# Optimization experiments

Measured on AMD Instinct MI355X. Metric: run time of the kernel, lower is better.

The kernel has to match this reference:

```python
import jax, jax.numpy as jnp
import numpy as np

N, D, L, K = 128, 512, 512, 512


def setup_inputs() -> dict:
    key = jax.random.key(0)
    k1, k2 = jax.random.split(key, 2)
    x = jax.random.normal(k1, (N, D, L), dtype=jnp.float32)
    a = jnp.ones((D,), dtype=jnp.float32) * 0.5
    sigma = jax.random.uniform(k2, (D,), dtype=jnp.float32)
    return {"x": x, "a": a, "sigma": sigma}


def reference(x, a, sigma):
    # x: (N, D, L); a, sigma: (D,)
    Lf = x.shape[-1]
    n = jnp.arange(Lf, dtype=x.dtype)                      # (L,)
    k = jnp.arange(K, dtype=x.dtype)                       # (K,)
    denom = jnp.asarray(Lf - 1, dtype=x.dtype)
    # Hann-family window per feature: w[d,l] = a[d] - (1-a[d]) cos(2*pi*l/(L-1))
    window = a[:, None] - (1.0 - a)[:, None] * jnp.cos(n * (2.0 * jnp.pi) / denom)  # (D, L)
    # windowed + sigma-scaled signal (fused elementwise)
    xw = x * (window * jnp.exp(sigma / denom)[:, None])    # (N, D, L)
    # complex DFT basis exp(j*2*pi*l*k/(L-1)) split into real/imag GEMMs
    ang = (2.0 * jnp.pi / denom) * (n[:, None] * k[None, :])  # (L, K)
    Xr = jnp.einsum('ndl,lk->ndk', xw, jnp.cos(ang))
    Xi = jnp.einsum('ndl,lk->ndk', xw, jnp.sin(ang))
    # abs_flag=True -> magnitude spectrum
    return jnp.sqrt(Xr * Xr + Xi * Xi)                     # (N, D, K)
```

## Files before the change

### kernel.cpp

```cpp
#include <hip/hip_runtime.h>
#include <hip/hip_bf16.h>
#include <math.h>

#define N_  128
#define D_  512
#define L_  512
#define K_  512
#define KH_ 256
#define M_  (N_*D_)

typedef __bf16 bf16x8 __attribute__((ext_vector_type(8)));
typedef float  f32x4  __attribute__((ext_vector_type(4)));
typedef unsigned short ushort_t;

__global__ void basis_kernel(const float* __restrict__ a,
                             const float* __restrict__ sigma,
                             ushort_t* __restrict__ Bc,
                             ushort_t* __restrict__ Bs,
                             float* __restrict__ P,
                             float* __restrict__ Q,
                             float* __restrict__ C) {
    int idx = blockIdx.x * 256 + threadIdx.x;
    int r = idx >> 9;
    int c = idx & 511;
    unsigned m = (unsigned)(r * c) % 511u;
    const float w0 = 6.283185307179586f / 511.0f;
    float sn, cs;
    sincosf((float)m * w0, &sn, &cs);
    __hip_bfloat16 bc = __float2bfloat16(cs);
    __hip_bfloat16 bs = __float2bfloat16(sn);
    ushort_t uc, us;
    __builtin_memcpy(&uc, &bc, 2);
    __builtin_memcpy(&us, &bs, 2);
    Bc[idx] = uc;
    Bs[idx] = us;
    if (idx < 512) {
        float e = expf(sigma[idx] * (1.0f / 511.0f));
        P[idx] = a[idx] * e;
        Q[idx] = -(1.0f - a[idx]) * e;
        C[idx] = cosf((float)idx * w0);
    }
}

static __device__ __forceinline__ unsigned pack_bf16x2(float lo, float hi) {
    __hip_bfloat162 h = __float22bfloat162_rn(make_float2(lo, hi));
    unsigned u;
    __builtin_memcpy(&u, &h, 4);
    return u;
}

__global__ __launch_bounds__(256, 2)
void dft_gemm6(const float* __restrict__ x,
               const ushort_t* __restrict__ Bc,
               const ushort_t* __restrict__ Bs,
               const float* __restrict__ P,
               const float* __restrict__ Q,
               const float* __restrict__ C,
               float* __restrict__ out) {
    const int tid  = threadIdx.x;
    const int w    = tid >> 6;
    const int lane = tid & 63;
    const int ml   = lane & 15;
    const int quad = lane >> 4;

    const int m0 = blockIdx.x * 64;
    const int n0 = w * 64;
    const int d0 = m0 & (D_ - 1);

    float p[4], q[4];
#pragma unroll
    for (int mi = 0; mi < 4; ++mi) {
        p[mi] = P[d0 + mi * 16 + ml];
        q[mi] = Q[d0 + mi * 16 + ml];
    }

    const float*    xb  = x  + (size_t)(m0 + ml) * L_ + quad * 8;
    const ushort_t* bcb = Bc + (size_t)(n0 + ml) * L_ + quad * 8;
    const ushort_t* bsb = Bs + (size_t)(n0 + ml) * L_ + quad * 8;
    const float*    Cb  = C  + quad * 8;

    f32x4 acc_c[4][4], acc_s[4][4];
    const f32x4 zero = {0.f, 0.f, 0.f, 0.f};
#pragma unroll
    for (int mi = 0; mi < 4; ++mi)
#pragma unroll
        for (int ni = 0; ni < 4; ++ni) { acc_c[mi][ni] = zero; acc_s[mi][ni] = zero; }

    for (int kk = 0; kk < L_; kk += 32) {
        float4 c0 = *(const float4*)(Cb + kk);
        float4 c1 = *(const float4*)(Cb + kk + 4);

        bf16x8 bcf[4], bsf[4];
#pragma unroll
        for (int ni = 0; ni < 4; ++ni) {
            bcf[ni] = *(const bf16x8*)(bcb + ni * (16 * L_) + kk);
            bsf[ni] = *(const bf16x8*)(bsb + ni * (16 * L_) + kk);
        }

        bf16x8 af[4];
#pragma unroll
        for (int mi = 0; mi < 4; ++mi) {
            float4 v0 = *(const float4*)(xb + mi * (16 * L_) + kk);
            float4 v1 = *(const float4*)(xb + mi * (16 * L_) + kk + 4);
            float w0 = fmaf(q[mi], c0.x, p[mi]);
            float w1 = fmaf(q[mi], c0.y, p[mi]);
            float w2 = fmaf(q[mi], c0.z, p[mi]);
            float w3 = fmaf(q[mi], c0.w, p[mi]);
            float w4 = fmaf(q[mi], c1.x, p[mi]);
            float w5 = fmaf(q[mi], c1.y, p[mi]);
            float w6 = fmaf(q[mi], c1.z, p[mi]);
            float w7 = fmaf(q[mi], c1.w, p[mi]);
            int4 pk;
            pk.x = (int)pack_bf16x2(v0.x * w0, v0.y * w1);
            pk.y = (int)pack_bf16x2(v0.z * w2, v0.w * w3);
            pk.z = (int)pack_bf16x2(v1.x * w4, v1.y * w5);
            pk.w = (int)pack_bf16x2(v1.z * w6, v1.w * w7);
            __builtin_memcpy(&af[mi], &pk, 16);
        }

#pragma unroll
        for (int mi = 0; mi < 4; ++mi)
#pragma unroll
            for (int ni = 0; ni < 4; ++ni) {
                acc_c[mi][ni] = __builtin_amdgcn_mfma_f32_16x16x32_bf16(
                    af[mi], bcf[ni], acc_c[mi][ni], 0, 0, 0);
                acc_s[mi][ni] = __builtin_amdgcn_mfma_f32_16x16x32_bf16(
                    af[mi], bsf[ni], acc_s[mi][ni], 0, 0, 0);
            }
    }

#pragma unroll
    for (int mi = 0; mi < 4; ++mi)
#pragma unroll
        for (int ni = 0; ni < 4; ++ni) {
#pragma unroll
            for (int r = 0; r < 4; ++r) {
                float cv = acc_c[mi][ni][r];
                float sv = acc_s[mi][ni][r];
                int row = m0 + mi * 16 + quad * 4 + r;
                int col = n0 + ni * 16 + ml;
                float v = sqrtf(cv * cv + sv * sv);
                out[(size_t)row * K_ + col] = v;
                out[(size_t)row * K_ + (K_ - 1 - col)] = v;
            }
        }
}

extern "C" void kernel_launch(void* const* d_in, const int* in_sizes, int n_in,
                              void* d_out, int out_size, void* d_ws, size_t ws_size,
                              hipStream_t stream) {
    (void)in_sizes; (void)n_in; (void)out_size; (void)ws_size;
    const float* x     = (const float*)d_in[0];
    const float* a     = (const float*)d_in[1];
    const float* sigma = (const float*)d_in[2];
    float* out = (float*)d_out;

    ushort_t* Bc = (ushort_t*)d_ws;
    ushort_t* Bs = Bc + KH_ * 512;
    float*    P  = (float*)(Bs + KH_ * 512);
    float*    Q  = P + 512;
    float*    C  = Q + 512;

    basis_kernel<<<dim3(512), dim3(256), 0, stream>>>(a, sigma, Bc, Bs, P, Q, C);
    dft_gemm6<<<dim3(1024), dim3(256), 0, stream>>>(x, Bc, Bs, P, Q, C, out);
}
```

Baseline: 328.7 us.

## Pre-swizzle DFT basis into MFMA fragment order and stage x through LDS

The basis kernel now writes the cosine/sine tables in a tiled layout that matches the MFMA B-fragment order, so each lane reads one contiguous 16-byte chunk per tile. In the GEMM, each wave loads x with a different thread mapping, windows it, packs it to bf16 and writes it into a per-wave double-buffered, XOR-swizzled LDS region, then reads A fragments back from LDS. Global x loads for the next k-tile are issued before the MFMAs on the current tile, and s_setprio is raised around the MFMA bursts. The intent is better coalescing and latency hiding in exchange for LDS traffic and extra register pressure. No barrier is needed because each wave only uses its own buffer.

```diff
diff --git a/kernel.cpp b/kernel.cpp
--- a/kernel.cpp
+++ b/kernel.cpp
@@ -32,8 +32,11 @@
     ushort_t uc, us;
     __builtin_memcpy(&uc, &bc, 2);
     __builtin_memcpy(&us, &bs, 2);
-    Bc[idx] = uc;
-    Bs[idx] = us;
+    int nb16 = r >> 4, ml = r & 15;
+    int kt = c >> 5, quad = (c >> 3) & 3, j = c & 7;
+    size_t pos = ((size_t)((nb16 * 16 + kt) * 64 + quad * 16 + ml)) * 8 + j;
+    Bc[pos] = uc;
+    Bs[pos] = us;
     if (idx < 512) {
         float e = expf(sigma[idx] * (1.0f / 511.0f));
         P[idx] = a[idx] * e;
@@ -50,13 +53,15 @@
 }
 
 __global__ __launch_bounds__(256, 2)
-void dft_gemm6(const float* __restrict__ x,
+void dft_gemm7(const float* __restrict__ x,
                const ushort_t* __restrict__ Bc,
                const ushort_t* __restrict__ Bs,
                const float* __restrict__ P,
                const float* __restrict__ Q,
                const float* __restrict__ C,
                float* __restrict__ out) {
+    __shared__ ushort_t sA[4 * 2 * 64 * 32];
+
     const int tid  = threadIdx.x;
     const int w    = tid >> 6;
     const int lane = tid & 63;
@@ -64,20 +69,38 @@
     const int quad = lane >> 4;
 
     const int m0 = blockIdx.x * 64;
+    const int d0 = m0 & (D_ - 1);
     const int n0 = w * 64;
-    const int d0 = m0 & (D_ - 1);
-
-    float p[4], q[4];
+
+    ushort_t* A0 = sA + w * 4096;
+    ushort_t* A1 = A0 + 2048;
+
+    const int rt = lane >> 2;
+    const int ct = lane & 3;
+
+    float pr[4], qr[4];
+#pragma unroll
+    for (int rb = 0; rb < 4; ++rb) {
+        pr[rb] = P[d0 + rb * 16 + rt];
+        qr[rb] = Q[d0 + rb * 16 + rt];
+    }
+    const float* xb = x + (size_t)(m0 + rt) * L_ + ct * 8;
+    const float* Cb = C + ct * 8;
+
+    int wOff[4];
+#pragma unroll
+    for (int rb = 0; rb < 4; ++rb) {
+        int row = rb * 16 + rt;
+        int pc  = ct ^ ((row >> 1) & 3);
+        wOff[rb] = row * 32 + pc * 8;
+    }
+    int aOff[4];
 #pragma unroll
     for (int mi = 0; mi < 4; ++mi) {
-        p[mi] = P[d0 + mi * 16 + ml];
-        q[mi] = Q[d0 + mi * 16 + ml];
-    }
-
-    const float*    xb  = x  + (size_t)(m0 + ml) * L_ + quad * 8;
-    const ushort_t* bcb = Bc + (size_t)(n0 + ml) * L_ + quad * 8;
-    const ushort_t* bsb = Bs + (size_t)(n0 + ml) * L_ + quad * 8;
-    const float*    Cb  = C  + quad * 8;
+        int ar = mi * 16 + ml;
+        int pc = quad ^ ((ar >> 1) & 3);
+        aOff[mi] = ar * 32 + pc * 8;
+    }
 
     f32x4 acc_c[4][4], acc_s[4][4];
     const f32x4 zero = {0.f, 0.f, 0.f, 0.f};
@@ -86,48 +109,73 @@
 #pragma unroll
         for (int ni = 0; ni < 4; ++ni) { acc_c[mi][ni] = zero; acc_s[mi][ni] = zero; }
 
-    for (int kk = 0; kk < L_; kk += 32) {
+    float4 xv[8];
+
+    auto xload = [&](int kk) {
+#pragma unroll
+        for (int rb = 0; rb < 4; ++rb) {
+            xv[2 * rb]     = *(const float4*)(xb + (size_t)rb * 16 * L_ + kk);
+            xv[2 * rb + 1] = *(const float4*)(xb + (size_t)rb * 16 * L_ + kk + 4);
+        }
+    };
+
+    auto packwrite = [&](int kk, ushort_t* Abuf) {
         float4 c0 = *(const float4*)(Cb + kk);
         float4 c1 = *(const float4*)(Cb + kk + 4);
-
-        bf16x8 bcf[4], bsf[4];
+#pragma unroll
+        for (int rb = 0; rb < 4; ++rb) {
+            float p = pr[rb], q = qr[rb];
+            float w0v = fmaf(q, c0.x, p), w1v = fmaf(q, c0.y, p);
+            float w2v = fmaf(q, c0.z, p), w3v = fmaf(q, c0.w, p);
+            float w4v = fmaf(q, c1.x, p), w5v = fmaf(q, c1.y, p);
+            float w6v = fmaf(q, c1.z, p), w7v = fmaf(q, c1.w, p);
+            float4 v0 = xv[2 * rb], v1 = xv[2 * rb + 1];
+            int4 pk;
+            pk.x = (int)pack_bf16x2(v0.x * w0v, v0.y * w1v);
+            pk.y = (int)pack_bf16x2(v0.z * w2v, v0.w * w3v);
+            pk.z = (int)pack_bf16x2(v1.x * w4v, v1.y * w5v);
+            pk.w = (int)pack_bf16x2(v1.z * w6v, v1.w * w7v);
+            *(int4*)(Abuf + wOff[rb]) = pk;
+        }
+    };
+
+    auto mfma_tile = [&](const ushort_t* Abuf, int kt) {
+        bf16x8 af[4];
+#pragma unroll
+        for (int mi = 0; mi < 4; ++mi)
+            af[mi] = *(const bf16x8*)(Abuf + aOff[mi]);
 #pragma unroll
         for (int ni = 0; ni < 4; ++ni) {
-            bcf[ni] = *(const bf16x8*)(bcb + ni * (16 * L_) + kk);
-            bsf[ni] = *(const bf16x8*)(bsb + ni * (16 * L_) + kk);
-        }
-
-        bf16x8 af[4];
-#pragma unroll
-        for (int mi = 0; mi < 4; ++mi) {
-            float4 v0 = *(const float4*)(xb + mi * (16 * L_) + kk);
-            float4 v1 = *(const float4*)(xb + mi * (16 * L_) + kk + 4);
-            float w0 = fmaf(q[mi], c0.x, p[mi]);
-            float w1 = fmaf(q[mi], c0.y, p[mi]);
-            float w2 = fmaf(q[mi], c0.z, p[mi]);
-            float w3 = fmaf(q[mi], c0.w, p[mi]);
-            float w4 = fmaf(q[mi], c1.x, p[mi]);
-            float w5 = fmaf(q[mi], c1.y, p[mi]);
-            float w6 = fmaf(q[mi], c1.z, p[mi]);
-            float w7 = fmaf(q[mi], c1.w, p[mi]);
-            int4 pk;
-            pk.x = (int)pack_bf16x2(v0.x * w0, v0.y * w1);
-            pk.y = (int)pack_bf16x2(v0.z * w2, v0.w * w3);
-            pk.z = (int)pack_bf16x2(v1.x * w4, v1.y * w5);
-            pk.w = (int)pack_bf16x2(v1.z * w6, v1.w * w7);
-            __builtin_memcpy(&af[mi], &pk, 16);
-        }
-
-#pragma unroll
-        for (int mi = 0; mi < 4; ++mi)
-#pragma unroll
-            for (int ni = 0; ni < 4; ++ni) {
+            const size_t tb = (((size_t)(w * 4 + ni) * 16 + kt) * 64 + lane) * 8;
+            bf16x8 bcf = *(const bf16x8*)(Bc + tb);
+            bf16x8 bsf = *(const bf16x8*)(Bs + tb);
+            __builtin_amdgcn_s_setprio(1);
+#pragma unroll
+            for (int mi = 0; mi < 4; ++mi) {
                 acc_c[mi][ni] = __builtin_amdgcn_mfma_f32_16x16x32_bf16(
-                    af[mi], bcf[ni], acc_c[mi][ni], 0, 0, 0);
+                    af[mi], bcf, acc_c[mi][ni], 0, 0, 0);
                 acc_s[mi][ni] = __builtin_amdgcn_mfma_f32_16x16x32_bf16(
-                    af[mi], bsf[ni], acc_s[mi][ni], 0, 0, 0);
+                    af[mi], bsf, acc_s[mi][ni], 0, 0, 0);
             }
-    }
+            __builtin_amdgcn_s_setprio(0);
+        }
+    };
+
+    xload(0);
+    packwrite(0, A0);
+#pragma unroll 1
+    for (int t = 0; t < 14; t += 2) {
+        xload((t + 1) * 32);
+        mfma_tile(A0, t);
+        packwrite((t + 1) * 32, A1);
+        xload((t + 2) * 32);
+        mfma_tile(A1, t + 1);
+        packwrite((t + 2) * 32, A0);
+    }
+    xload(15 * 32);
+    mfma_tile(A0, 14);
+    packwrite(15 * 32, A1);
+    mfma_tile(A1, 15);
 
 #pragma unroll
     for (int mi = 0; mi < 4; ++mi)
@@ -162,5 +210,5 @@
     float*    C  = Q + 512;
 
     basis_kernel<<<dim3(512), dim3(256), 0, stream>>>(a, sigma, Bc, Bs, P, Q, C);
-    dft_gemm6<<<dim3(1024), dim3(256), 0, stream>>>(x, Bc, Bs, P, Q, C, out);
-}
+    dft_gemm7<<<dim3(1024), dim3(256), 0, stream>>>(x, Bc, Bs, P, Q, C, out);
+}
```

Measured after the change: 281.8 us. 1.17x faster.

## Stage A and basis tiles through double-buffered LDS with direct global-to-LDS loads

Applied to the files above, without the earlier changes.

Replaces the per-wave direct global loads with cooperative global_load_lds staging of the x tile and both basis tiles into double-buffered, XOR-swizzled shared memory, so each x row is loaded once per block instead of once per wave. The block tile becomes 64x128 output columns with each wave covering 32 columns, so there are twice as many blocks, remapped so neighbouring blocks are grouped differently. Launch bounds move to 3 blocks per CU. The cost is added LDS traffic and barriers, and each x tile is now reloaded by two blocks.

```diff
diff --git a/kernel.cpp b/kernel.cpp
--- a/kernel.cpp
+++ b/kernel.cpp
@@ -49,96 +49,155 @@
     return u;
 }
 
-__global__ __launch_bounds__(256, 2)
-void dft_gemm6(const float* __restrict__ x,
+static __device__ __forceinline__ void load_lds_128(const void* g, void* l) {
+    __builtin_amdgcn_global_load_lds(
+        (const __attribute__((address_space(1))) unsigned int*)g,
+        (__attribute__((address_space(3))) unsigned int*)l,
+        16, 0, 0);
+}
+
+__global__ __launch_bounds__(256, 3)
+void dft_gemm8(const float* __restrict__ x,
                const ushort_t* __restrict__ Bc,
                const ushort_t* __restrict__ Bs,
                const float* __restrict__ P,
                const float* __restrict__ Q,
                const float* __restrict__ C,
                float* __restrict__ out) {
+    __shared__ float    sA [2 * 64 * 32];
+    __shared__ ushort_t sBc[2 * 128 * 32];
+    __shared__ ushort_t sBs[2 * 128 * 32];
+
+    const int b  = blockIdx.x;
+    const int wg = (b & 7) * 256 + (b >> 3);
+    const int ng = wg & 1;
+    const int mg = wg >> 1;
+    const int m0 = mg * 64;
+    const int n0 = ng * 128;
+    const int d0 = m0 & (D_ - 1);
+
     const int tid  = threadIdx.x;
     const int w    = tid >> 6;
     const int lane = tid & 63;
     const int ml   = lane & 15;
     const int quad = lane >> 4;
 
-    const int m0 = blockIdx.x * 64;
-    const int n0 = w * 64;
-    const int d0 = m0 & (D_ - 1);
-
-    float p[4], q[4];
+    const int arA = tid >> 3;
+    const int pcA = tid & 7;
+    const int lcA = pcA ^ (arA & 7);
+    const float* aS0 = x + (size_t)(m0 + arA) * L_ + lcA * 4;
+    const float* aS1 = x + (size_t)(m0 + 32 + arA) * L_ + lcA * 4;
+
+    const int brB = tid >> 2;
+    const int bqB = (tid & 3) ^ ((brB >> 1) & 3);
+    const ushort_t* bcS0 = Bc + (size_t)(n0 + brB) * L_ + bqB * 8;
+    const ushort_t* bcS1 = Bc + (size_t)(n0 + 64 + brB) * L_ + bqB * 8;
+    const ushort_t* bsS0 = Bs + (size_t)(n0 + brB) * L_ + bqB * 8;
+    const ushort_t* bsS1 = Bs + (size_t)(n0 + 64 + brB) * L_ + bqB * 8;
+
+    int aOff0[4], aOff1[4];
 #pragma unroll
     for (int mi = 0; mi < 4; ++mi) {
-        p[mi] = P[d0 + mi * 16 + ml];
-        q[mi] = Q[d0 + mi * 16 + ml];
-    }
-
-    const float*    xb  = x  + (size_t)(m0 + ml) * L_ + quad * 8;
-    const ushort_t* bcb = Bc + (size_t)(n0 + ml) * L_ + quad * 8;
-    const ushort_t* bsb = Bs + (size_t)(n0 + ml) * L_ + quad * 8;
-    const float*    Cb  = C  + quad * 8;
-
-    f32x4 acc_c[4][4], acc_s[4][4];
+        int ar = mi * 16 + ml;
+        int s  = ar & 7;
+        aOff0[mi] = ar * 32 + ((2 * quad) ^ s) * 4;
+        aOff1[mi] = ar * 32 + ((2 * quad + 1) ^ s) * 4;
+    }
+    int bOff[2];
+#pragma unroll
+    for (int ni = 0; ni < 2; ++ni) {
+        int br = w * 32 + ni * 16 + ml;
+        int pc = quad ^ ((br >> 1) & 3);
+        bOff[ni] = br * 32 + pc * 8;
+    }
+
+    float pa[4], qa[4];
+#pragma unroll
+    for (int mi = 0; mi < 4; ++mi) {
+        pa[mi] = P[d0 + mi * 16 + ml];
+        qa[mi] = Q[d0 + mi * 16 + ml];
+    }
+    const float* Cq = C + quad * 8;
+
+    f32x4 acc_c[4][2], acc_s[4][2];
     const f32x4 zero = {0.f, 0.f, 0.f, 0.f};
 #pragma unroll
     for (int mi = 0; mi < 4; ++mi)
 #pragma unroll
-        for (int ni = 0; ni < 4; ++ni) { acc_c[mi][ni] = zero; acc_s[mi][ni] = zero; }
-
-    for (int kk = 0; kk < L_; kk += 32) {
-        float4 c0 = *(const float4*)(Cb + kk);
-        float4 c1 = *(const float4*)(Cb + kk + 4);
-
-        bf16x8 bcf[4], bsf[4];
-#pragma unroll
-        for (int ni = 0; ni < 4; ++ni) {
-            bcf[ni] = *(const bf16x8*)(bcb + ni * (16 * L_) + kk);
-            bsf[ni] = *(const bf16x8*)(bsb + ni * (16 * L_) + kk);
-        }
-
+        for (int ni = 0; ni < 2; ++ni) { acc_c[mi][ni] = zero; acc_s[mi][ni] = zero; }
+
+#define STAGE(buf, kk)                                                        \
+    do {                                                                      \
+        const int fo_ = (buf) * 2048;                            \
+        const int uo_ = (buf) * 4096;                            \
+        load_lds_128(aS0  + (kk), sA  + fo_ + w * 256);                       \
+        load_lds_128(aS1  + (kk), sA  + fo_ + 1024 + w * 256);                \
+        load_lds_128(bcS0 + (kk), sBc + uo_ + w * 512);                       \
+        load_lds_128(bcS1 + (kk), sBc + uo_ + 2048 + w * 512);                \
+        load_lds_128(bsS0 + (kk), sBs + uo_ + w * 512);                       \
+        load_lds_128(bsS1 + (kk), sBs + uo_ + 2048 + w * 512);                \
+    } while (0)
+
+    auto compute_tile = [&](int buf, int kk) {
+        const int fo = buf * 2048;
+        const int uo = buf * 4096;
+        float4 cv0 = *(const float4*)(Cq + kk);
+        float4 cv1 = *(const float4*)(Cq + kk + 4);
         bf16x8 af[4];
 #pragma unroll
         for (int mi = 0; mi < 4; ++mi) {
-            float4 v0 = *(const float4*)(xb + mi * (16 * L_) + kk);
-            float4 v1 = *(const float4*)(xb + mi * (16 * L_) + kk + 4);
-            float w0 = fmaf(q[mi], c0.x, p[mi]);
-            float w1 = fmaf(q[mi], c0.y, p[mi]);
-            float w2 = fmaf(q[mi], c0.z, p[mi]);
-            float w3 = fmaf(q[mi], c0.w, p[mi]);
-            float w4 = fmaf(q[mi], c1.x, p[mi]);
-            float w5 = fmaf(q[mi], c1.y, p[mi]);
-            float w6 = fmaf(q[mi], c1.z, p[mi]);
-            float w7 = fmaf(q[mi], c1.w, p[mi]);
+            float4 f0 = *(const float4*)&sA[fo + aOff0[mi]];
+            float4 f1 = *(const float4*)&sA[fo + aOff1[mi]];
+            float p = pa[mi], q = qa[mi];
             int4 pk;
-            pk.x = (int)pack_bf16x2(v0.x * w0, v0.y * w1);
-            pk.y = (int)pack_bf16x2(v0.z * w2, v0.w * w3);
-            pk.z = (int)pack_bf16x2(v1.x * w4, v1.y * w5);
-            pk.w = (int)pack_bf16x2(v1.z * w6, v1.w * w7);
+            pk.x = (int)pack_bf16x2(f0.x * fmaf(q, cv0.x, p),
+                                    f0.y * fmaf(q, cv0.y, p));
+            pk.y = (int)pack_bf16x2(f0.z * fmaf(q, cv0.z, p),
+                                    f0.w * fmaf(q, cv0.w, p));
+            pk.z = (int)pack_bf16x2(f1.x * fmaf(q, cv1.x, p),
+                                    f1.y * fmaf(q, cv1.y, p));
+            pk.w = (int)pack_bf16x2(f1.z * fmaf(q, cv1.z, p),
+                                    f1.w * fmaf(q, cv1.w, p));
             __builtin_memcpy(&af[mi], &pk, 16);
         }
-
-#pragma unroll
-        for (int mi = 0; mi < 4; ++mi)
-#pragma unroll
-            for (int ni = 0; ni < 4; ++ni) {
+#pragma unroll
+        for (int ni = 0; ni < 2; ++ni) {
+            bf16x8 bcf = *(const bf16x8*)&sBc[uo + bOff[ni]];
+            bf16x8 bsf = *(const bf16x8*)&sBs[uo + bOff[ni]];
+#pragma unroll
+            for (int mi = 0; mi < 4; ++mi) {
                 acc_c[mi][ni] = __builtin_amdgcn_mfma_f32_16x16x32_bf16(
-                    af[mi], bcf[ni], acc_c[mi][ni], 0, 0, 0);
+                    af[mi], bcf, acc_c[mi][ni], 0, 0, 0);
                 acc_s[mi][ni] = __builtin_amdgcn_mfma_f32_16x16x32_bf16(
-                    af[mi], bsf[ni], acc_s[mi][ni], 0, 0, 0);
+                    af[mi], bsf, acc_s[mi][ni], 0, 0, 0);
             }
-    }
+        }
+    };
+
+    STAGE(0, 0);
+    __syncthreads();
+
+    int cur = 0;
+    for (int kk = 32; kk < L_; kk += 32) {
+        STAGE(cur ^ 1, kk);
+        compute_tile(cur, kk - 32);
+        __syncthreads();
+        cur ^= 1;
+    }
+    compute_tile(cur, L_ - 32);
+
+#undef STAGE
 
 #pragma unroll
     for (int mi = 0; mi < 4; ++mi)
 #pragma unroll
-        for (int ni = 0; ni < 4; ++ni) {
+        for (int ni = 0; ni < 2; ++ni) {
 #pragma unroll
             for (int r = 0; r < 4; ++r) {
                 float cv = acc_c[mi][ni][r];
                 float sv = acc_s[mi][ni][r];
                 int row = m0 + mi * 16 + quad * 4 + r;
-                int col = n0 + ni * 16 + ml;
+                int col = n0 + w * 32 + ni * 16 + ml;
                 float v = sqrtf(cv * cv + sv * sv);
                 out[(size_t)row * K_ + col] = v;
                 out[(size_t)row * K_ + (K_ - 1 - col)] = v;
@@ -162,5 +221,5 @@
     float*    C  = Q + 512;
 
     basis_kernel<<<dim3(512), dim3(256), 0, stream>>>(a, sigma, Bc, Bs, P, Q, C);
-    dft_gemm6<<<dim3(1024), dim3(256), 0, stream>>>(x, Bc, Bs, P, Q, C, out);
-}
+    dft_gemm8<<<dim3(2048), dim3(256), 0, stream>>>(x, Bc, Bs, P, Q, C, out);
+}
```

New measurement: 299.4 us. -8.9%, faster.
